# Kernel optimization log

Measured on AMD Instinct MI355X. Metric: run time of the kernel, lower is better.

Reference implementation:

```python
import jax, jax.numpy as jnp
import numpy as np

U = 100000  # num_users
I = 100000  # num_items
D = 64      # dims
L = 50      # seq_L


def setup_inputs() -> dict:
    key = jax.random.key(0)
    ks = jax.random.split(key, 12)
    B, T = 4096, 100
    inp = {
        "user_ids": jax.random.randint(ks[0], (B,), 0, U),
        "item_seq_ids": jax.random.randint(ks[1], (B, L), 0, I),
        "target_item_ids": jax.random.randint(ks[2], (B, T), 0, I),
        # embedding tables (normal init)
        "user_table": jax.random.normal(ks[3], (U, D), jnp.float32) * 0.01,
        "item_table": jax.random.normal(ks[4], (I, D), jnp.float32) * 0.01,
        "W2_table": jax.random.normal(ks[5], (I, D), jnp.float32) * 0.01,
        "b2_table": jnp.zeros((I, 1), jnp.float32),
        # feature gates: Linear(dims, dims), he_uniform weight, zero bias
        "fg_item_W": jax.random.uniform(ks[6], (D, D), jnp.float32, -1.0, 1.0) * np.sqrt(6.0 / D),
        "fg_item_b": jnp.zeros((D,), jnp.float32),
        "fg_user_W": jax.random.uniform(ks[7], (D, D), jnp.float32, -1.0, 1.0) * np.sqrt(6.0 / D),
        "fg_user_b": jnp.zeros((D,), jnp.float32),
        # instance gates: xavier_uniform
        "inst_gate_item": jax.random.uniform(ks[8], (D, 1), jnp.float32, -1.0, 1.0) * np.sqrt(6.0 / (D + 1)),
        "inst_gate_user": jax.random.uniform(ks[9], (D, L), jnp.float32, -1.0, 1.0) * np.sqrt(6.0 / (D + L)),
    }
    return inp


def _forward_user(user_emb, item_embs, fg_item_W, fg_item_b, fg_user_W, fg_user_b,
                  inst_gate_item, inst_gate_user):
    # user_emb: [B,D], item_embs: [B,L,D]
    gate = jax.nn.sigmoid(
        item_embs @ fg_item_W.T + fg_item_b
        + (user_emb @ fg_user_W.T + fg_user_b)[:, None, :]
    )  # [B,L,D]
    gated = item_embs * gate  # [B,L,D]
    term1 = jnp.einsum("bld,d->bl", gated, inst_gate_item[:, 0])
    term2 = user_emb @ inst_gate_user  # [B,L]
    inst = jax.nn.sigmoid(term1 + term2)  # [B,L]
    union = jnp.sum(gated * inst[:, :, None], axis=1)  # [B,D]
    union = union / jnp.sum(inst, axis=1, keepdims=True)
    return union


def reference(user_ids, item_seq_ids, target_item_ids, user_table, item_table,
              W2_table, b2_table, fg_item_W, fg_item_b, fg_user_W, fg_user_b,
              inst_gate_item, inst_gate_user):
    item_embs = item_table[item_seq_ids]      # [B,L,D]
    user_emb = user_table[user_ids]           # [B,D]
    union = _forward_user(user_emb, item_embs, fg_item_W, fg_item_b,
                          fg_user_W, fg_user_b, inst_gate_item, inst_gate_user)
    w2 = W2_table[target_item_ids]            # [B,T,D]
    b2 = b2_table[target_item_ids][..., 0]    # [B,T]
    res = b2 + jnp.einsum("btd,bd->bt", w2, user_emb)
    res = res + jnp.einsum("bd,btd->bt", union, w2)
    # rel_score: bmm(item_embs, w2^T) summed over L == contract item_embs summed over L with w2
    res = res + jnp.einsum("bd,btd->bt", jnp.sum(item_embs, axis=1), w2)
    return res
```

## Files before the change

kernel.cpp:

```cpp
#include <hip/hip_runtime.h>

#define DD 64
#define LL 50
#define NB 4096
#define NT 100

typedef __attribute__((ext_vector_type(8))) __bf16 bf16x8;
typedef __attribute__((ext_vector_type(4))) float f32x4;

__device__ __forceinline__ float sigmoidf_(float x) {
    return 1.0f / (1.0f + __expf(-x));
}
__device__ __forceinline__ float b2f(unsigned short h) {
    union { unsigned int u; float f; } v; v.u = ((unsigned int)h) << 16; return v.f;
}
__device__ __forceinline__ unsigned pack_bf16(float hi, float lo) {
    union { float f; unsigned u; } a, b;
    a.f = hi; b.f = lo;
    return ((a.u + 0x8000u) & 0xffff0000u) | ((b.u + 0x8000u) >> 16);
}
__device__ __forceinline__ uint4 cvt8u(const float* f) {
    uint4 r;
    r.x = pack_bf16(f[1], f[0]);
    r.y = pack_bf16(f[3], f[2]);
    r.z = pack_bf16(f[5], f[4]);
    r.w = pack_bf16(f[7], f[6]);
    return r;
}
__device__ __forceinline__ bf16x8 cvt8(const float* f) {
    return __builtin_bit_cast(bf16x8, cvt8u(f));
}

__global__ __launch_bounds__(64) void k0_user(
    const int* __restrict__ uid_g, const float* __restrict__ user_table,
    const float* __restrict__ Wu, const float* __restrict__ bu,
    const float* __restrict__ bi, const float* __restrict__ igu,
    float* __restrict__ ufg_ws, float* __restrict__ t2_ws)
{
    const int lane = threadIdx.x;
    const int c = lane & 15, q = lane >> 4;
    const int uid = uid_g[blockIdx.x * 16 + c];
    const float* urow = user_table + (size_t)uid * DD;

    bf16x8 af[2];
#pragma unroll
    for (int kf = 0; kf < 2; kf++) {
        float tmp[8];
        *(float4*)&tmp[0] = *(const float4*)(urow + kf * 32 + q * 8);
        *(float4*)&tmp[4] = *(const float4*)(urow + kf * 32 + q * 8 + 4);
        af[kf] = cvt8(tmp);
    }

#pragma unroll
    for (int ni = 0; ni < 8; ni++) {
        f32x4 a = {0.f, 0.f, 0.f, 0.f};
#pragma unroll
        for (int kf = 0; kf < 2; kf++) {
            const int k0 = kf * 32 + q * 8;
            float tmp[8];
            if (ni < 4) {
                const float* src = Wu + (ni * 16 + c) * DD + k0;
                *(float4*)&tmp[0] = *(const float4*)src;
                *(float4*)&tmp[4] = *(const float4*)(src + 4);
            } else {
                const int l = ni * 16 + c - 64;
#pragma unroll
                for (int j = 0; j < 8; j++)
                    tmp[j] = (l < LL) ? igu[(k0 + j) * LL + l] : 0.f;
            }
            a = __builtin_amdgcn_mfma_f32_16x16x32_bf16(af[kf], cvt8(tmp), a, 0, 0, 0);
        }
        const int n = ni * 16 + c;
#pragma unroll
        for (int reg = 0; reg < 4; reg++) {
            const int bo = blockIdx.x * 16 + q * 4 + reg;
            if (n < DD)           ufg_ws[bo * DD + n] = a[reg] + bu[n] + bi[n];
            else if (n < DD + LL) t2_ws[bo * DD + (n - DD)] = a[reg];
        }
    }
}

__global__ __launch_bounds__(256) void k1_union(
    const int* __restrict__ uid_g, const int* __restrict__ iid_g,
    const float* __restrict__ user_table, const float* __restrict__ item_table,
    const float* __restrict__ Wi, const float* __restrict__ igi,
    const float* __restrict__ ufg_ws, const float* __restrict__ t2_ws,
    float* __restrict__ v_ws)
{
    const int tid = threadIdx.x;
    const int w = tid >> 6, lane = tid & 63;
    const int c = lane & 15, q = lane >> 4;
    const int b = blockIdx.x * 4 + w;

    __shared__ unsigned short sE[4][LL][72];
    __shared__ unsigned short sW[DD][72];
    __shared__ float sT[4][DD];

    {
        const int n = tid >> 2, ch = tid & 3;
        float tmp[16];
        const float* src = Wi + n * DD + ch * 16;
        *(float4*)&tmp[0]  = *(const float4*)(src);
        *(float4*)&tmp[4]  = *(const float4*)(src + 4);
        *(float4*)&tmp[8]  = *(const float4*)(src + 8);
        *(float4*)&tmp[12] = *(const float4*)(src + 12);
        *(uint4*)&sW[n][ch * 16]     = cvt8u(tmp);
        *(uint4*)&sW[n][ch * 16 + 8] = cvt8u(tmp + 8);
    }

    sT[w][lane] = t2_ws[b * DD + lane];

    const int* iid = iid_g + b * LL;
    bf16x8 ea[4][2];
#pragma unroll
    for (int mi = 0; mi < 4; mi++) {
        const int l = mi * 16 + c;
        if (l < LL) {
            const float* src = item_table + (size_t)iid[l] * DD;
#pragma unroll
            for (int kf = 0; kf < 2; kf++) {
                float tmp[8];
                *(float4*)&tmp[0] = *(const float4*)(src + kf * 32 + q * 8);
                *(float4*)&tmp[4] = *(const float4*)(src + kf * 32 + q * 8 + 4);
                uint4 p = cvt8u(tmp);
                ea[mi][kf] = __builtin_bit_cast(bf16x8, p);
                *(uint4*)&sE[w][l][kf * 32 + q * 8] = p;
            }
        } else {
            uint4 z = {0u, 0u, 0u, 0u};
            ea[mi][0] = __builtin_bit_cast(bf16x8, z);
            ea[mi][1] = __builtin_bit_cast(bf16x8, z);
        }
    }
    __syncthreads();

    bf16x8 wb[4][2];
#pragma unroll
    for (int ni = 0; ni < 4; ni++)
#pragma unroll
        for (int kf = 0; kf < 2; kf++)
            wb[ni][kf] = __builtin_bit_cast(bf16x8,
                *(const uint4*)&sW[ni * 16 + c][kf * 32 + q * 8]);

    float ufg4[4], igi4[4];
#pragma unroll
    for (int ni = 0; ni < 4; ni++) {
        ufg4[ni] = ufg_ws[b * DD + ni * 16 + c];
        igi4[ni] = igi[ni * 16 + c];
    }

    float unum[4] = {0.f, 0.f, 0.f, 0.f};
    float sip[4]  = {0.f, 0.f, 0.f, 0.f};
    float isum = 0.f;

#pragma unroll
    for (int mi = 0; mi < 4; mi++) {
        f32x4 acc[4];
#pragma unroll
        for (int ni = 0; ni < 4; ni++) {
            f32x4 a = {0.f, 0.f, 0.f, 0.f};
            a = __builtin_amdgcn_mfma_f32_16x16x32_bf16(ea[mi][0], wb[ni][0], a, 0, 0, 0);
            a = __builtin_amdgcn_mfma_f32_16x16x32_bf16(ea[mi][1], wb[ni][1], a, 0, 0, 0);
            acc[ni] = a;
        }
        float gated[4][4], inst_r[4];
#pragma unroll
        for (int reg = 0; reg < 4; reg++) {
            const int l = mi * 16 + q * 4 + reg;
            const int valid = (l < LL);
            const int lc = valid ? l : 0;
            const float lm = valid ? 1.f : 0.f;
            float t1 = 0.f;
#pragma unroll
            for (int ni = 0; ni < 4; ni++) {
                const float e = b2f(sE[w][lc][ni * 16 + c]) * lm;
                const float g = sigmoidf_(acc[ni][reg] + ufg4[ni]);
                const float gd = e * g;
                gated[reg][ni] = gd;
                t1 += gd * igi4[ni];
                sip[ni] += e;
            }
            t1 += __shfl_xor(t1, 1); t1 += __shfl_xor(t1, 2);
            t1 += __shfl_xor(t1, 4); t1 += __shfl_xor(t1, 8);
            inst_r[reg] = valid ? sigmoidf_(t1 + sT[w][lc]) : 0.f;
        }
#pragma unroll
        for (int reg = 0; reg < 4; reg++) {
            isum += inst_r[reg];
#pragma unroll
            for (int ni = 0; ni < 4; ni++)
                unum[ni] += gated[reg][ni] * inst_r[reg];
        }
    }

#pragma unroll
    for (int ni = 0; ni < 4; ni++) {
        unum[ni] += __shfl_xor(unum[ni], 16); unum[ni] += __shfl_xor(unum[ni], 32);
        sip[ni]  += __shfl_xor(sip[ni], 16);  sip[ni]  += __shfl_xor(sip[ni], 32);
    }
    isum += __shfl_xor(isum, 16); isum += __shfl_xor(isum, 32);

    const float un = (q == 0) ? unum[0] : (q == 1) ? unum[1] : (q == 2) ? unum[2] : unum[3];
    const float si = (q == 0) ? sip[0]  : (q == 1) ? sip[1]  : (q == 2) ? sip[2]  : sip[3];
    const int uid = uid_g[b];
    const float u = user_table[(size_t)uid * DD + lane];
    v_ws[b * DD + lane] = u + un / isum + si;
}

__global__ __launch_bounds__(256) void k2_score(
    const int* __restrict__ tgt_g, const float* __restrict__ W2,
    const float* __restrict__ b2, const float* __restrict__ v_ws,
    float* __restrict__ out)
{
    const int b = blockIdx.x;
    const int tid = threadIdx.x;
    __shared__ float sv[DD];
    __shared__ int sids[NT];
    __shared__ float sout[NT + 12];

    if (tid < DD) sv[tid] = v_ws[b * DD + tid];
    if (tid < NT) sids[tid] = tgt_g[b * NT + tid];
    __syncthreads();

    const int j = tid & 15, g = tid >> 4;
    float4 vr = *(const float4*)&sv[j * 4];

#pragma unroll
    for (int it = 0; it < 7; it++) {
        const int t = it * 16 + g;
        if (t < NT) {
            const int id = sids[t];
            float4 wv = *(const float4*)(W2 + (size_t)id * DD + j * 4);
            float s = wv.x * vr.x + wv.y * vr.y + wv.z * vr.z + wv.w * vr.w;
            s += __shfl_xor(s, 1);
            s += __shfl_xor(s, 2);
            s += __shfl_xor(s, 4);
            s += __shfl_xor(s, 8);
            if (j == 0) sout[t] = s + b2[id];
        }
    }
    __syncthreads();
    if (tid < NT) out[b * NT + tid] = sout[tid];
}

extern "C" void kernel_launch(void* const* d_in, const int* in_sizes, int n_in,
                              void* d_out, int out_size, void* d_ws, size_t ws_size,
                              hipStream_t stream)
{
    const int* user_ids        = (const int*)d_in[0];
    const int* item_seq_ids    = (const int*)d_in[1];
    const int* target_item_ids = (const int*)d_in[2];
    const float* user_tab      = (const float*)d_in[3];
    const float* item_tab      = (const float*)d_in[4];
    const float* W2_tab        = (const float*)d_in[5];
    const float* b2_tab        = (const float*)d_in[6];
    const float* fg_item_W     = (const float*)d_in[7];
    const float* fg_item_b     = (const float*)d_in[8];
    const float* fg_user_W     = (const float*)d_in[9];
    const float* fg_user_b     = (const float*)d_in[10];
    const float* igi           = (const float*)d_in[11];
    const float* igu           = (const float*)d_in[12];
    float* out = (float*)d_out;

    float* ufg_ws = (float*)d_ws;
    float* t2_ws  = ufg_ws + NB * DD;
    float* v_ws   = t2_ws + NB * DD;

    k0_user<<<NB / 16, 64, 0, stream>>>(user_ids, user_tab, fg_user_W,
                                        fg_user_b, fg_item_b, igu, ufg_ws, t2_ws);
    k1_union<<<NB / 4, 256, 0, stream>>>(user_ids, item_seq_ids, user_tab,
                                         item_tab, fg_item_W, igi, ufg_ws,
                                         t2_ws, v_ws);
    k2_score<<<NB, 256, 0, stream>>>(target_item_ids, W2_tab, b2_tab, v_ws, out);
}
```

Baseline: 161.1 us.

## Fuse scoring kernel into union kernel and drop shared weight staging

```diff
diff --git a/kernel.cpp b/kernel.cpp
--- a/kernel.cpp
+++ b/kernel.cpp
@@ -80,12 +80,14 @@
     }
 }
 
-__global__ __launch_bounds__(256) void k1_union(
+__global__ __launch_bounds__(256) void k1_fused(
     const int* __restrict__ uid_g, const int* __restrict__ iid_g,
+    const int* __restrict__ tgt_g,
     const float* __restrict__ user_table, const float* __restrict__ item_table,
+    const float* __restrict__ W2, const float* __restrict__ b2,
     const float* __restrict__ Wi, const float* __restrict__ igi,
     const float* __restrict__ ufg_ws, const float* __restrict__ t2_ws,
-    float* __restrict__ v_ws)
+    float* __restrict__ out)
 {
     const int tid = threadIdx.x;
     const int w = tid >> 6, lane = tid & 63;
@@ -93,20 +95,14 @@
     const int b = blockIdx.x * 4 + w;
 
     __shared__ unsigned short sE[4][LL][72];
-    __shared__ unsigned short sW[DD][72];
     __shared__ float sT[4][DD];
-
-    {
-        const int n = tid >> 2, ch = tid & 3;
-        float tmp[16];
-        const float* src = Wi + n * DD + ch * 16;
-        *(float4*)&tmp[0]  = *(const float4*)(src);
-        *(float4*)&tmp[4]  = *(const float4*)(src + 4);
-        *(float4*)&tmp[8]  = *(const float4*)(src + 8);
-        *(float4*)&tmp[12] = *(const float4*)(src + 12);
-        *(uint4*)&sW[n][ch * 16]     = cvt8u(tmp);
-        *(uint4*)&sW[n][ch * 16 + 8] = cvt8u(tmp + 8);
-    }
+    __shared__ int   sids[4][NT];
+    __shared__ float sv4[4][DD];
+    __shared__ float sout[4][NT];
+
+    const int* tb = tgt_g + b * NT;
+    sids[w][lane] = tb[lane];
+    if (lane < NT - 64) sids[w][64 + lane] = tb[64 + lane];
 
     sT[w][lane] = t2_ws[b * DD + lane];
 
@@ -132,15 +128,18 @@
             ea[mi][1] = __builtin_bit_cast(bf16x8, z);
         }
     }
-    __syncthreads();
 
     bf16x8 wb[4][2];
 #pragma unroll
     for (int ni = 0; ni < 4; ni++)
 #pragma unroll
-        for (int kf = 0; kf < 2; kf++)
-            wb[ni][kf] = __builtin_bit_cast(bf16x8,
-                *(const uint4*)&sW[ni * 16 + c][kf * 32 + q * 8]);
+        for (int kf = 0; kf < 2; kf++) {
+            float tmp[8];
+            const float* src = Wi + (ni * 16 + c) * DD + kf * 32 + q * 8;
+            *(float4*)&tmp[0] = *(const float4*)src;
+            *(float4*)&tmp[4] = *(const float4*)(src + 4);
+            wb[ni][kf] = cvt8(tmp);
+        }
 
     float ufg4[4], igi4[4];
 #pragma unroll
@@ -204,43 +203,26 @@
     const float si = (q == 0) ? sip[0]  : (q == 1) ? sip[1]  : (q == 2) ? sip[2]  : sip[3];
     const int uid = uid_g[b];
     const float u = user_table[(size_t)uid * DD + lane];
-    v_ws[b * DD + lane] = u + un / isum + si;
-}
-
-__global__ __launch_bounds__(256) void k2_score(
-    const int* __restrict__ tgt_g, const float* __restrict__ W2,
-    const float* __restrict__ b2, const float* __restrict__ v_ws,
-    float* __restrict__ out)
-{
-    const int b = blockIdx.x;
-    const int tid = threadIdx.x;
-    __shared__ float sv[DD];
-    __shared__ int sids[NT];
-    __shared__ float sout[NT + 12];
-
-    if (tid < DD) sv[tid] = v_ws[b * DD + tid];
-    if (tid < NT) sids[tid] = tgt_g[b * NT + tid];
-    __syncthreads();
-
-    const int j = tid & 15, g = tid >> 4;
-    float4 vr = *(const float4*)&sv[j * 4];
-
-#pragma unroll
-    for (int it = 0; it < 7; it++) {
-        const int t = it * 16 + g;
-        if (t < NT) {
-            const int id = sids[t];
-            float4 wv = *(const float4*)(W2 + (size_t)id * DD + j * 4);
-            float s = wv.x * vr.x + wv.y * vr.y + wv.z * vr.z + wv.w * vr.w;
-            s += __shfl_xor(s, 1);
-            s += __shfl_xor(s, 2);
-            s += __shfl_xor(s, 4);
-            s += __shfl_xor(s, 8);
-            if (j == 0) sout[t] = s + b2[id];
-        }
-    }
-    __syncthreads();
-    if (tid < NT) out[b * NT + tid] = sout[tid];
+    sv4[w][lane] = u + un / isum + si;
+
+    const int j = lane & 15, g2 = lane >> 4;
+    float4 vr = *(const float4*)&sv4[w][j * 4];
+
+#pragma unroll 5
+    for (int i = 0; i < 25; i++) {
+        const int t = i * 4 + g2;
+        const int id = sids[w][t];
+        float4 wv = *(const float4*)(W2 + (size_t)id * DD + j * 4);
+        float s = wv.x * vr.x + wv.y * vr.y + wv.z * vr.z + wv.w * vr.w;
+        s += __shfl_xor(s, 1);
+        s += __shfl_xor(s, 2);
+        s += __shfl_xor(s, 4);
+        s += __shfl_xor(s, 8);
+        if (j == 0) sout[w][t] = s + b2[id];
+    }
+
+    out[b * NT + lane] = sout[w][lane];
+    if (lane < NT - 64) out[b * NT + 64 + lane] = sout[w][64 + lane];
 }
 
 extern "C" void kernel_launch(void* const* d_in, const int* in_sizes, int n_in,
@@ -264,12 +246,10 @@
 
     float* ufg_ws = (float*)d_ws;
     float* t2_ws  = ufg_ws + NB * DD;
-    float* v_ws   = t2_ws + NB * DD;
 
     k0_user<<<NB / 16, 64, 0, stream>>>(user_ids, user_tab, fg_user_W,
                                         fg_user_b, fg_item_b, igu, ufg_ws, t2_ws);
-    k1_union<<<NB / 4, 256, 0, stream>>>(user_ids, item_seq_ids, user_tab,
-                                         item_tab, fg_item_W, igi, ufg_ws,
-                                         t2_ws, v_ws);
-    k2_score<<<NB, 256, 0, stream>>>(target_item_ids, W2_tab, b2_tab, v_ws, out);
-}
+    k1_fused<<<NB / 4, 256, 0, stream>>>(user_ids, item_seq_ids, target_item_ids,
+                                         user_tab, item_tab, W2_tab, b2_tab,
+                                         fg_item_W, igi, ufg_ws, t2_ws, out);
+}
```

Result: slower. 184.3 us (+14.4%).

## Split each union sequence across two waves and load gate weights directly

Applied to the files above, without the earlier changes.

```diff
diff --git a/kernel.cpp b/kernel.cpp
--- a/kernel.cpp
+++ b/kernel.cpp
@@ -89,32 +89,24 @@
 {
     const int tid = threadIdx.x;
     const int w = tid >> 6, lane = tid & 63;
+    const int p = w >> 1, h = w & 1;
     const int c = lane & 15, q = lane >> 4;
-    const int b = blockIdx.x * 4 + w;
-
-    __shared__ unsigned short sE[4][LL][72];
-    __shared__ unsigned short sW[DD][72];
-    __shared__ float sT[4][DD];
-
-    {
-        const int n = tid >> 2, ch = tid & 3;
-        float tmp[16];
-        const float* src = Wi + n * DD + ch * 16;
-        *(float4*)&tmp[0]  = *(const float4*)(src);
-        *(float4*)&tmp[4]  = *(const float4*)(src + 4);
-        *(float4*)&tmp[8]  = *(const float4*)(src + 8);
-        *(float4*)&tmp[12] = *(const float4*)(src + 12);
-        *(uint4*)&sW[n][ch * 16]     = cvt8u(tmp);
-        *(uint4*)&sW[n][ch * 16 + 8] = cvt8u(tmp + 8);
-    }
-
-    sT[w][lane] = t2_ws[b * DD + lane];
+    const int b = blockIdx.x * 2 + p;
+
+    __shared__ unsigned short sE[4][32][72];
+    __shared__ float sT[2][DD];
+    __shared__ float sU[4][DD];
+    __shared__ float sS[4][DD];
+    __shared__ float sI[4];
+
+    if (h == 0) sT[p][lane] = t2_ws[b * DD + lane];
 
     const int* iid = iid_g + b * LL;
-    bf16x8 ea[4][2];
-#pragma unroll
-    for (int mi = 0; mi < 4; mi++) {
-        const int l = mi * 16 + c;
+    bf16x8 ea[2][2];
+#pragma unroll
+    for (int mi = 0; mi < 2; mi++) {
+        const int r = mi * 16 + c;
+        const int l = 32 * h + r;
         if (l < LL) {
             const float* src = item_table + (size_t)iid[l] * DD;
 #pragma unroll
@@ -122,9 +114,9 @@
                 float tmp[8];
                 *(float4*)&tmp[0] = *(const float4*)(src + kf * 32 + q * 8);
                 *(float4*)&tmp[4] = *(const float4*)(src + kf * 32 + q * 8 + 4);
-                uint4 p = cvt8u(tmp);
-                ea[mi][kf] = __builtin_bit_cast(bf16x8, p);
-                *(uint4*)&sE[w][l][kf * 32 + q * 8] = p;
+                uint4 pk = cvt8u(tmp);
+                ea[mi][kf] = __builtin_bit_cast(bf16x8, pk);
+                *(uint4*)&sE[w][r][kf * 32 + q * 8] = pk;
             }
         } else {
             uint4 z = {0u, 0u, 0u, 0u};
@@ -132,15 +124,18 @@
             ea[mi][1] = __builtin_bit_cast(bf16x8, z);
         }
     }
-    __syncthreads();
 
     bf16x8 wb[4][2];
 #pragma unroll
     for (int ni = 0; ni < 4; ni++)
 #pragma unroll
-        for (int kf = 0; kf < 2; kf++)
-            wb[ni][kf] = __builtin_bit_cast(bf16x8,
-                *(const uint4*)&sW[ni * 16 + c][kf * 32 + q * 8]);
+        for (int kf = 0; kf < 2; kf++) {
+            float tmp[8];
+            const float* src = Wi + (ni * 16 + c) * DD + kf * 32 + q * 8;
+            *(float4*)&tmp[0] = *(const float4*)src;
+            *(float4*)&tmp[4] = *(const float4*)(src + 4);
+            wb[ni][kf] = cvt8(tmp);
+        }
 
     float ufg4[4], igi4[4];
 #pragma unroll
@@ -153,8 +148,10 @@
     float sip[4]  = {0.f, 0.f, 0.f, 0.f};
     float isum = 0.f;
 
-#pragma unroll
-    for (int mi = 0; mi < 4; mi++) {
+    __syncthreads();
+
+#pragma unroll
+    for (int mi = 0; mi < 2; mi++) {
         f32x4 acc[4];
 #pragma unroll
         for (int ni = 0; ni < 4; ni++) {
@@ -166,14 +163,15 @@
         float gated[4][4], inst_r[4];
 #pragma unroll
         for (int reg = 0; reg < 4; reg++) {
-            const int l = mi * 16 + q * 4 + reg;
+            const int r = mi * 16 + q * 4 + reg;
+            const int l = 32 * h + r;
             const int valid = (l < LL);
-            const int lc = valid ? l : 0;
             const float lm = valid ? 1.f : 0.f;
+            const int rc = valid ? r : 0;
             float t1 = 0.f;
 #pragma unroll
             for (int ni = 0; ni < 4; ni++) {
-                const float e = b2f(sE[w][lc][ni * 16 + c]) * lm;
+                const float e = b2f(sE[w][rc][ni * 16 + c]) * lm;
                 const float g = sigmoidf_(acc[ni][reg] + ufg4[ni]);
                 const float gd = e * g;
                 gated[reg][ni] = gd;
@@ -182,7 +180,7 @@
             }
             t1 += __shfl_xor(t1, 1); t1 += __shfl_xor(t1, 2);
             t1 += __shfl_xor(t1, 4); t1 += __shfl_xor(t1, 8);
-            inst_r[reg] = valid ? sigmoidf_(t1 + sT[w][lc]) : 0.f;
+            inst_r[reg] = valid ? sigmoidf_(t1 + sT[p][32 * h + rc]) : 0.f;
         }
 #pragma unroll
         for (int reg = 0; reg < 4; reg++) {
@@ -202,9 +200,20 @@
 
     const float un = (q == 0) ? unum[0] : (q == 1) ? unum[1] : (q == 2) ? unum[2] : unum[3];
     const float si = (q == 0) ? sip[0]  : (q == 1) ? sip[1]  : (q == 2) ? sip[2]  : sip[3];
-    const int uid = uid_g[b];
-    const float u = user_table[(size_t)uid * DD + lane];
-    v_ws[b * DD + lane] = u + un / isum + si;
+    sU[w][lane] = un;
+    sS[w][lane] = si;
+    if (lane == 0) sI[w] = isum;
+    __syncthreads();
+
+    if (h == 0) {
+        const int d = lane;
+        const float num = sU[2 * p][d] + sU[2 * p + 1][d];
+        const float ss  = sS[2 * p][d] + sS[2 * p + 1][d];
+        const float den = sI[2 * p] + sI[2 * p + 1];
+        const int uid = uid_g[b];
+        const float u = user_table[(size_t)uid * DD + d];
+        v_ws[b * DD + d] = u + num / den + ss;
+    }
 }
 
 __global__ __launch_bounds__(256) void k2_score(
@@ -268,7 +277,7 @@
 
     k0_user<<<NB / 16, 64, 0, stream>>>(user_ids, user_tab, fg_user_W,
                                         fg_user_b, fg_item_b, igu, ufg_ws, t2_ws);
-    k1_union<<<NB / 4, 256, 0, stream>>>(user_ids, item_seq_ids, user_tab,
+    k1_union<<<NB / 2, 256, 0, stream>>>(user_ids, item_seq_ids, user_tab,
                                          item_tab, fg_item_W, igi, ufg_ws,
                                          t2_ws, v_ws);
     k2_score<<<NB, 256, 0, stream>>>(target_item_ids, W2_tab, b2_tab, v_ws, out);
```

After: 170.2 us. 1.06x slower.

## Stage item gathers via global_load_lds, precompute bf16 Wi, batch W2 loads

Applied to the files above, without the earlier changes.

```diff
diff --git a/kernel.cpp b/kernel.cpp
--- a/kernel.cpp
+++ b/kernel.cpp
@@ -10,9 +10,6 @@
 
 __device__ __forceinline__ float sigmoidf_(float x) {
     return 1.0f / (1.0f + __expf(-x));
-}
-__device__ __forceinline__ float b2f(unsigned short h) {
-    union { unsigned int u; float f; } v; v.u = ((unsigned int)h) << 16; return v.f;
 }
 __device__ __forceinline__ unsigned pack_bf16(float hi, float lo) {
     union { float f; unsigned u; } a, b;
@@ -30,13 +27,37 @@
 __device__ __forceinline__ bf16x8 cvt8(const float* f) {
     return __builtin_bit_cast(bf16x8, cvt8u(f));
 }
+__device__ __forceinline__ void glds16(const float* g, float* l) {
+    __builtin_amdgcn_global_load_lds(
+        (const __attribute__((address_space(1))) void*)g,
+        (__attribute__((address_space(3))) void*)l, 16, 0, 0);
+}
+__device__ __forceinline__ void glds4(const float* g, float* l) {
+    __builtin_amdgcn_global_load_lds(
+        (const __attribute__((address_space(1))) void*)g,
+        (__attribute__((address_space(3))) void*)l, 4, 0, 0);
+}
 
 __global__ __launch_bounds__(64) void k0_user(
     const int* __restrict__ uid_g, const float* __restrict__ user_table,
     const float* __restrict__ Wu, const float* __restrict__ bu,
     const float* __restrict__ bi, const float* __restrict__ igu,
-    float* __restrict__ ufg_ws, float* __restrict__ t2_ws)
+    const float* __restrict__ Wi,
+    float* __restrict__ ufg_ws, float* __restrict__ t2_ws,
+    unsigned short* __restrict__ wiB_ws)
 {
+    if (blockIdx.x == 256) {
+        const int n = threadIdx.x;
+        float tmp[64];
+#pragma unroll
+        for (int c4 = 0; c4 < 16; c4++)
+            *(float4*)&tmp[c4 * 4] = *(const float4*)(Wi + n * DD + c4 * 4);
+#pragma unroll
+        for (int ch = 0; ch < 8; ch++)
+            *(uint4*)(wiB_ws + n * DD + ch * 8) = cvt8u(tmp + ch * 8);
+        return;
+    }
+
     const int lane = threadIdx.x;
     const int c = lane & 15, q = lane >> 4;
     const int uid = uid_g[blockIdx.x * 16 + c];
@@ -80,59 +101,35 @@
     }
 }
 
-__global__ __launch_bounds__(256) void k1_union(
+__global__ __launch_bounds__(64) void k1_union(
     const int* __restrict__ uid_g, const int* __restrict__ iid_g,
     const float* __restrict__ user_table, const float* __restrict__ item_table,
-    const float* __restrict__ Wi, const float* __restrict__ igi,
+    const unsigned short* __restrict__ wiB, const float* __restrict__ igi,
     const float* __restrict__ ufg_ws, const float* __restrict__ t2_ws,
     float* __restrict__ v_ws)
 {
-    const int tid = threadIdx.x;
-    const int w = tid >> 6, lane = tid & 63;
+    const int lane = threadIdx.x;
     const int c = lane & 15, q = lane >> 4;
-    const int b = blockIdx.x * 4 + w;
-
-    __shared__ unsigned short sE[4][LL][72];
-    __shared__ unsigned short sW[DD][72];
-    __shared__ float sT[4][DD];
-
-    {
-        const int n = tid >> 2, ch = tid & 3;
-        float tmp[16];
-        const float* src = Wi + n * DD + ch * 16;
-        *(float4*)&tmp[0]  = *(const float4*)(src);
-        *(float4*)&tmp[4]  = *(const float4*)(src + 4);
-        *(float4*)&tmp[8]  = *(const float4*)(src + 8);
-        *(float4*)&tmp[12] = *(const float4*)(src + 12);
-        *(uint4*)&sW[n][ch * 16]     = cvt8u(tmp);
-        *(uint4*)&sW[n][ch * 16 + 8] = cvt8u(tmp + 8);
-    }
-
-    sT[w][lane] = t2_ws[b * DD + lane];
-
-    const int* iid = iid_g + b * LL;
-    bf16x8 ea[4][2];
-#pragma unroll
-    for (int mi = 0; mi < 4; mi++) {
-        const int l = mi * 16 + c;
-        if (l < LL) {
-            const float* src = item_table + (size_t)iid[l] * DD;
-#pragma unroll
-            for (int kf = 0; kf < 2; kf++) {
-                float tmp[8];
-                *(float4*)&tmp[0] = *(const float4*)(src + kf * 32 + q * 8);
-                *(float4*)&tmp[4] = *(const float4*)(src + kf * 32 + q * 8 + 4);
-                uint4 p = cvt8u(tmp);
-                ea[mi][kf] = __builtin_bit_cast(bf16x8, p);
-                *(uint4*)&sE[w][l][kf * 32 + q * 8] = p;
-            }
-        } else {
-            uint4 z = {0u, 0u, 0u, 0u};
-            ea[mi][0] = __builtin_bit_cast(bf16x8, z);
-            ea[mi][1] = __builtin_bit_cast(bf16x8, z);
-        }
-    }
-    __syncthreads();
+    const int b = blockIdx.x;
+
+    __shared__ __align__(16) float sE[52 * DD + DD];
+    float* sT = sE + 52 * DD;
+
+    const int* iidp = iid_g + b * LL;
+    int ids[13];
+#pragma unroll
+    for (int s = 0; s < 13; s++) {
+        const int r = 4 * s + (lane >> 4);
+        ids[s] = iidp[r < LL ? r : LL - 1];
+    }
+
+#pragma unroll
+    for (int s = 0; s < 13; s++) {
+        const int r = 4 * s + (lane >> 4);
+        const int j = (lane & 15) ^ (r & 7);
+        glds16(item_table + (size_t)ids[s] * DD + j * 4, sE + s * 256);
+    }
+    glds4(t2_ws + b * DD + (lane < LL ? lane : LL - 1), sT);
 
     bf16x8 wb[4][2];
 #pragma unroll
@@ -140,13 +137,39 @@
 #pragma unroll
         for (int kf = 0; kf < 2; kf++)
             wb[ni][kf] = __builtin_bit_cast(bf16x8,
-                *(const uint4*)&sW[ni * 16 + c][kf * 32 + q * 8]);
+                *(const uint4*)(wiB + (ni * 16 + c) * DD + kf * 32 + q * 8));
 
     float ufg4[4], igi4[4];
 #pragma unroll
     for (int ni = 0; ni < 4; ni++) {
         ufg4[ni] = ufg_ws[b * DD + ni * 16 + c];
         igi4[ni] = igi[ni * 16 + c];
+    }
+    const int uid = uid_g[b];
+    const float u = user_table[(size_t)uid * DD + lane];
+
+    __syncthreads();
+
+    bf16x8 ea[4][2];
+#pragma unroll
+    for (int mi = 0; mi < 4; mi++) {
+        const int row = mi * 16 + c;
+        const int rr = (row < LL) ? row : 0;
+        const float* rowp = sE + rr * DD;
+        const int s7 = rr & 7;
+#pragma unroll
+        for (int kf = 0; kf < 2; kf++) {
+            float tmp[8];
+            const int ch0 = (kf * 8 + 2 * q) ^ s7;
+            const int ch1 = (kf * 8 + 2 * q + 1) ^ s7;
+            *(float4*)&tmp[0] = *(const float4*)(rowp + ch0 * 4);
+            *(float4*)&tmp[4] = *(const float4*)(rowp + ch1 * 4);
+            if (row >= LL) {
+#pragma unroll
+                for (int i = 0; i < 8; i++) tmp[i] = 0.f;
+            }
+            ea[mi][kf] = cvt8(tmp);
+        }
     }
 
     float unum[4] = {0.f, 0.f, 0.f, 0.f};
@@ -168,12 +191,14 @@
         for (int reg = 0; reg < 4; reg++) {
             const int l = mi * 16 + q * 4 + reg;
             const int valid = (l < LL);
-            const int lc = valid ? l : 0;
-            const float lm = valid ? 1.f : 0.f;
+            const int lr = valid ? l : 0;
+            const int s7 = lr & 7;
             float t1 = 0.f;
 #pragma unroll
             for (int ni = 0; ni < 4; ni++) {
-                const float e = b2f(sE[w][lc][ni * 16 + c]) * lm;
+                const int phys = (4 * ni + (c >> 2)) ^ s7;
+                const float ev = sE[lr * DD + phys * 4 + (c & 3)];
+                const float e = valid ? ev : 0.f;
                 const float g = sigmoidf_(acc[ni][reg] + ufg4[ni]);
                 const float gd = e * g;
                 gated[reg][ni] = gd;
@@ -182,7 +207,7 @@
             }
             t1 += __shfl_xor(t1, 1); t1 += __shfl_xor(t1, 2);
             t1 += __shfl_xor(t1, 4); t1 += __shfl_xor(t1, 8);
-            inst_r[reg] = valid ? sigmoidf_(t1 + sT[w][lc]) : 0.f;
+            inst_r[reg] = valid ? sigmoidf_(t1 + sT[lr]) : 0.f;
         }
 #pragma unroll
         for (int reg = 0; reg < 4; reg++) {
@@ -202,8 +227,6 @@
 
     const float un = (q == 0) ? unum[0] : (q == 1) ? unum[1] : (q == 2) ? unum[2] : unum[3];
     const float si = (q == 0) ? sip[0]  : (q == 1) ? sip[1]  : (q == 2) ? sip[2]  : sip[3];
-    const int uid = uid_g[b];
-    const float u = user_table[(size_t)uid * DD + lane];
     v_ws[b * DD + lane] = u + un / isum + si;
 }
 
@@ -215,29 +238,36 @@
     const int b = blockIdx.x;
     const int tid = threadIdx.x;
     __shared__ float sv[DD];
-    __shared__ int sids[NT];
-    __shared__ float sout[NT + 12];
+    __shared__ int sids[112];
+    __shared__ float sout[112];
 
     if (tid < DD) sv[tid] = v_ws[b * DD + tid];
-    if (tid < NT) sids[tid] = tgt_g[b * NT + tid];
+    if (tid < 112) {
+        const int t = (tid < NT) ? tid : NT - 1;
+        sids[tid] = tgt_g[b * NT + t];
+    }
     __syncthreads();
 
     const int j = tid & 15, g = tid >> 4;
     float4 vr = *(const float4*)&sv[j * 4];
 
-#pragma unroll
-    for (int it = 0; it < 7; it++) {
-        const int t = it * 16 + g;
-        if (t < NT) {
-            const int id = sids[t];
-            float4 wv = *(const float4*)(W2 + (size_t)id * DD + j * 4);
-            float s = wv.x * vr.x + wv.y * vr.y + wv.z * vr.z + wv.w * vr.w;
-            s += __shfl_xor(s, 1);
-            s += __shfl_xor(s, 2);
-            s += __shfl_xor(s, 4);
-            s += __shfl_xor(s, 8);
-            if (j == 0) sout[t] = s + b2[id];
-        }
+    int id[7];
+#pragma unroll
+    for (int i = 0; i < 7; i++) id[i] = sids[i * 16 + g];
+    float4 wv[7];
+#pragma unroll
+    for (int i = 0; i < 7; i++)
+        wv[i] = *(const float4*)(W2 + (size_t)id[i] * DD + j * 4);
+    float bb[7];
+#pragma unroll
+    for (int i = 0; i < 7; i++) bb[i] = b2[id[i]];
+
+#pragma unroll
+    for (int i = 0; i < 7; i++) {
+        float s = wv[i].x * vr.x + wv[i].y * vr.y + wv[i].z * vr.z + wv[i].w * vr.w;
+        s += __shfl_xor(s, 1); s += __shfl_xor(s, 2);
+        s += __shfl_xor(s, 4); s += __shfl_xor(s, 8);
+        if (j == 0) sout[i * 16 + g] = s + bb[i];
     }
     __syncthreads();
     if (tid < NT) out[b * NT + tid] = sout[tid];
@@ -265,11 +295,12 @@
     float* ufg_ws = (float*)d_ws;
     float* t2_ws  = ufg_ws + NB * DD;
     float* v_ws   = t2_ws + NB * DD;
-
-    k0_user<<<NB / 16, 64, 0, stream>>>(user_ids, user_tab, fg_user_W,
-                                        fg_user_b, fg_item_b, igu, ufg_ws, t2_ws);
-    k1_union<<<NB / 4, 256, 0, stream>>>(user_ids, item_seq_ids, user_tab,
-                                         item_tab, fg_item_W, igi, ufg_ws,
-                                         t2_ws, v_ws);
+    unsigned short* wiB_ws = (unsigned short*)(v_ws + NB * DD);
+
+    k0_user<<<257, 64, 0, stream>>>(user_ids, user_tab, fg_user_W, fg_user_b,
+                                    fg_item_b, igu, fg_item_W,
+                                    ufg_ws, t2_ws, wiB_ws);
+    k1_union<<<NB, 64, 0, stream>>>(user_ids, item_seq_ids, user_tab, item_tab,
+                                    wiB_ws, igi, ufg_ws, t2_ws, v_ws);
     k2_score<<<NB, 256, 0, stream>>>(target_item_ids, W2_tab, b2_tab, v_ws, out);
 }
```

Measured after the change: 159.4 us. About the same (-1.0%).
